# Optimization experiments

Hardware: AMD Instinct MI355X
Metric: run time of the kernel (lower is better)

## Reference

```python
import jax, jax.numpy as jnp
import numpy as np

B, T, C, H = 2, 2048, 2048, 32
N = C // H  # 64
EPS_GN = 1e-5 * 8 ** 2  # eps = 1e-5 * head_size_divisor**2


def setup_inputs() -> dict:
    key = jax.random.key(0)
    ks = jax.random.split(key, 40)
    p = lambda i, shape, s=1.0: jax.random.normal(ks[i], shape, jnp.float32) * s
    inp = {
        'x': p(0, (B, T, C)),
        'shift_state': jnp.zeros((B, C), jnp.float32),
        'v_first': p(1, (B, T, C)),
        'wkv_state': jnp.zeros((B, H, N, N), jnp.float32),
        # token-shift mix coefficients [1,1,C]
        'x_r': p(2, (1, 1, C), 0.3), 'x_w': p(3, (1, 1, C), 0.3),
        'x_k': p(4, (1, 1, C), 0.3), 'x_v': p(5, (1, 1, C), 0.3),
        'x_a': p(6, (1, 1, C), 0.3), 'x_g': p(7, (1, 1, C), 0.3),
        # decay LoRA
        'w0': p(8, (1, 1, C), 0.5) - 4.0,
        'w1': p(9, (C, 64), 0.02), 'w2': p(10, (64, C), 0.02),
        # in-context-learning-rate LoRA
        'a0': p(11, (1, 1, C), 0.1),
        'a1': p(12, (C, 64), 0.02), 'a2': p(13, (64, C), 0.02),
        # value-mix LoRA
        'v0': p(14, (1, 1, C), 0.1) + 1.0,
        'v1': p(15, (C, 32), 0.02), 'v2': p(16, (32, C), 0.02),
        # gate LoRA
        'g1': p(17, (C, 128), 0.02), 'g2': p(18, (128, C), 0.02),
        'k_k': p(19, (1, 1, C), 0.05) + 0.85,
        'k_a': p(20, (1, 1, C), 0.05) + 1.0,
        'r_k': p(21, (H, N), 0.1),
        # dense projections (applied as x @ W.T like nn.Linear)
        'Wr': p(22, (C, C), 0.02), 'Wk': p(23, (C, C), 0.02),
        'Wv': p(24, (C, C), 0.02), 'Wo': p(25, (C, C), 0.02),
        'ln_w': jnp.ones((C,), jnp.float32),
        'ln_b': jnp.zeros((C,), jnp.float32),
    }
    return inp


def reference(x, shift_state, v_first, wkv_state, x_r, x_w, x_k, x_v, x_a, x_g,
              w0, w1, w2, a0, a1, a2, v0, v1, v2, g1, g2, k_k, k_a, r_k,
              Wr, Wk, Wv, Wo, ln_w, ln_b):
    # token shift: xx[t] = x[t-1] - x[t] (prev from shift_state at t=0)
    xx = jnp.concatenate([shift_state[:, None, :], x[:, :-1]], axis=1) - x
    xr, xw, xk, xv, xa, xg = (x + xx * m for m in (x_r, x_w, x_k, x_v, x_a, x_g))

    r = xr @ Wr.T
    w = -jax.nn.softplus(-(w0 + jnp.tanh(xw @ w1) @ w2)) - 0.5  # log-decay in (-inf,-0.5)
    k = xk @ Wk.T
    v = xv @ Wv.T
    v = v + (v_first - v) * jax.nn.sigmoid(v0 + (xv @ v1) @ v2)  # layer_id > 0 branch
    a = jax.nn.sigmoid(a0 + (xa @ a1) @ a2)
    g = jax.nn.sigmoid(xg @ g1) @ g2

    kk = (k * k_k).reshape(B, T, H, N)
    kk = kk / jnp.maximum(jnp.linalg.norm(kk, axis=-1, keepdims=True), 1e-12)
    kk = kk.reshape(B, T, C)
    k = k * (1.0 + (a - 1.0) * k_a)

    # RWKV-7 generalized delta-rule recurrence (a_in=-kk, b_in=kk*a):
    #   S_t = S_{t-1} * diag(exp(w_t)) + (S_{t-1} a_t) b_t^T + v_t k_t^T ; o_t = S_t r_t
    to_tbhn = lambda z: z.reshape(B, T, H, N).transpose(1, 0, 2, 3)  # [T,B,H,N]
    rs, ws, ks, vs, as_, bs = map(to_tbhn, (r, w, k, v, -kk, kk * a))

    def step(S, ins):  # S: [B,H,N,N] indexed [v_dim, k_dim]
        r_t, w_t, k_t, v_t, a_t, b_t = ins
        sa = jnp.einsum('bhij,bhj->bhi', S, a_t)
        S = (S * jnp.exp(w_t)[:, :, None, :]
             + sa[..., None] * b_t[:, :, None, :]
             + v_t[..., None] * k_t[:, :, None, :])
        o_t = jnp.einsum('bhij,bhj->bhi', S, r_t)
        return S, o_t

    _, o = jax.lax.scan(step, wkv_state, (rs, ws, ks, vs, as_, bs))  # o: [T,B,H,N]
    o = o.transpose(1, 0, 2, 3).reshape(B, T, C)

    # GroupNorm with H groups over channel dim
    og = o.reshape(B, T, H, N)
    mu = og.mean(-1, keepdims=True)
    var = og.var(-1, keepdims=True)
    o = ((og - mu) / jnp.sqrt(var + EPS_GN)).reshape(B, T, C) * ln_w + ln_b

    # bonus term
    rk = (r.reshape(B, T, H, N) * k.reshape(B, T, H, N) * r_k).sum(-1, keepdims=True)
    o = o + (rk * v.reshape(B, T, H, N)).reshape(B, T, C)

    return (o * g) @ Wo.T
```

## Files before the change

kernel.cpp:

```cpp
#include <hip/hip_runtime.h>

#define Bdim 2
#define Tdim 2048
#define Cdim 2048
#define Hdim 32
#define Mdim (Bdim*Tdim)

typedef unsigned short u16;
typedef short bf16x8 __attribute__((ext_vector_type(8)));
typedef float f32x2 __attribute__((ext_vector_type(2)));
typedef float f32x4 __attribute__((ext_vector_type(4)));

__device__ __forceinline__ u16 f2bf(float f) {
  unsigned u = __float_as_uint(f);
  u = (u + 0x7FFFu + ((u >> 16) & 1u)) >> 16;
  return (u16)u;
}
__device__ __forceinline__ float b2f(u16 h) {
  return __uint_as_float(((unsigned)h) << 16);
}
__device__ __forceinline__ float sigf(float x) { return 1.f / (1.f + expf(-x)); }

__device__ __forceinline__ void gld16(const u16* g, u16* l) {
  __builtin_amdgcn_global_load_lds(
      (const __attribute__((address_space(1))) unsigned int*)g,
      (__attribute__((address_space(3))) unsigned int*)l, 16, 0, 0);
}

__device__ __forceinline__ float dpp_red16(float x) {
  int t = __builtin_amdgcn_mov_dpp(__float_as_int(x), 0x128, 0xF, 0xF, true);
  x += __int_as_float(t);
  t = __builtin_amdgcn_mov_dpp(__float_as_int(x), 0x124, 0xF, 0xF, true);
  x += __int_as_float(t);
  t = __builtin_amdgcn_mov_dpp(__float_as_int(x), 0x122, 0xF, 0xF, true);
  x += __int_as_float(t);
  t = __builtin_amdgcn_mov_dpp(__float_as_int(x), 0x121, 0xF, 0xF, true);
  x += __int_as_float(t);
  return x;
}

__global__ __launch_bounds__(256) void fill_kernel(float* __restrict__ out, float v, int n) {
  int i = blockIdx.x * 256 + threadIdx.x;
  if (i < n) out[i] = v;
}

__global__ __launch_bounds__(256) void prep_kernel(
    const float* __restrict__ x, const float* __restrict__ shift,
    const float* __restrict__ mr, const float* __restrict__ mw,
    const float* __restrict__ mk, const float* __restrict__ mv,
    const float* __restrict__ ma, const float* __restrict__ mg,
    u16* __restrict__ xr_h, u16* __restrict__ xr_l,
    u16* __restrict__ xk_h, u16* __restrict__ xk_l,
    u16* __restrict__ xv_h, u16* __restrict__ xv_l,
    u16* __restrict__ xg_h, u16* __restrict__ xg_l,
    u16* __restrict__ xw, u16* __restrict__ xa)
{
  size_t idx = (size_t)blockIdx.x * 256 + threadIdx.x;
  int c = (int)(idx & (Cdim - 1));
  size_t row = idx >> 11;
  int t = (int)(row & (Tdim - 1));
  int b = (int)(row >> 11);
  float xc = x[idx];
  float xp = (t == 0) ? shift[(size_t)b * Cdim + c] : x[idx - Cdim];
  float xx = xp - xc;

  float vr = xc + xx * mr[c];
  u16 hr = f2bf(vr); xr_h[idx] = hr; xr_l[idx] = f2bf(vr - b2f(hr));
  float vk = xc + xx * mk[c];
  u16 hk = f2bf(vk); xk_h[idx] = hk; xk_l[idx] = f2bf(vk - b2f(hk));
  float vv = xc + xx * mv[c];
  u16 hv = f2bf(vv); xv_h[idx] = hv; xv_l[idx] = f2bf(vv - b2f(hv));
  float vg = xc + xx * mg[c];
  u16 hg = f2bf(vg); xg_h[idx] = hg; xg_l[idx] = f2bf(vg - b2f(hg));

  xw[idx] = f2bf(xc + xx * mw[c]);
  xa[idx] = f2bf(xc + xx * ma[c]);
}

__global__ __launch_bounds__(256) void cast_split_kernel(
    const float* __restrict__ src, u16* __restrict__ hi, u16* __restrict__ lo)
{
  size_t i = (size_t)blockIdx.x * 256 + threadIdx.x;
  float v = src[i];
  u16 h = f2bf(v);
  hi[i] = h;
  lo[i] = f2bf(v - b2f(h));
}

__global__ __launch_bounds__(256) void pack_all_kernel(
    const float* __restrict__ w1, const float* __restrict__ a1,
    const float* __restrict__ v1, const float* __restrict__ g1,
    const float* __restrict__ w2, const float* __restrict__ a2,
    const float* __restrict__ v2, const float* __restrict__ g2,
    u16* __restrict__ w1t, u16* __restrict__ a1t, u16* __restrict__ v1t,
    u16* __restrict__ g1t_h, u16* __restrict__ g1t_l,
    u16* __restrict__ w2t, u16* __restrict__ a2t, u16* __restrict__ v2t,
    u16* __restrict__ g2t_h, u16* __restrict__ g2t_l)
{
  int bid = blockIdx.x;
  const float* src; u16* dh; u16* dl = nullptr;
  int K, Nsrc; size_t idx0;
  if (bid < 1024)      { src = w1; dh = w1t;   K = 2048; Nsrc = 64;   idx0 = (size_t)bid * 256; }
  else if (bid < 2048) { src = a1; dh = a1t;   K = 2048; Nsrc = 64;   idx0 = (size_t)(bid - 1024) * 256; }
  else if (bid < 3072) { src = v1; dh = v1t;   K = 2048; Nsrc = 32;   idx0 = (size_t)(bid - 2048) * 256; }
  else if (bid < 4096) { src = g1; dh = g1t_h; dl = g1t_l; K = 2048; Nsrc = 128; idx0 = (size_t)(bid - 3072) * 256; }
  else if (bid < 4608) { src = w2; dh = w2t;   K = 64;   Nsrc = 2048; idx0 = (size_t)(bid - 4096) * 256; }
  else if (bid < 5120) { src = a2; dh = a2t;   K = 64;   Nsrc = 2048; idx0 = (size_t)(bid - 4608) * 256; }
  else if (bid < 5376) { src = v2; dh = v2t;   K = 32;   Nsrc = 2048; idx0 = (size_t)(bid - 5120) * 256; }
  else                 { src = g2; dh = g2t_h; dl = g2t_l; K = 128;  Nsrc = 2048; idx0 = (size_t)(bid - 5376) * 256; }
  size_t idx = idx0 + threadIdx.x;
  int n = (int)(idx / K);
  int kk = (int)(idx - (size_t)n * K);
  float v = (n < Nsrc) ? src[(size_t)kk * Nsrc + n] : 0.f;
  u16 h = f2bf(v);
  dh[idx] = h;
  if (dl) dl[idx] = f2bf(v - b2f(h));
}


template <int EP>
__device__ __forceinline__ void gemm_plain_body(
    const u16* __restrict__ A, const u16* __restrict__ B, void* __restrict__ Cv,
    const float* __restrict__ bias, const float* __restrict__ aux1,
    const float* __restrict__ aux2, int K, int Nact, int ldC, int act)
{
  __shared__ u16 As[2][128][32];
  __shared__ u16 Bs[2][128][32];
  int tid = threadIdx.x;
  int lane = tid & 63, wave = tid >> 6;
  int wm = wave >> 1, wn = wave & 1;
  int bm = blockIdx.x * 128, bn = blockIdx.y * 128;
  f32x4 zero = {0.f, 0.f, 0.f, 0.f};
  f32x4 acc[4][4];
#pragma unroll
  for (int i = 0; i < 4; i++)
#pragma unroll
    for (int j = 0; j < 4; j++) acc[i][j] = zero;
  int srow = tid >> 2;
  int sslot = tid & 3;
  int scol = (sslot ^ (srow & 3)) << 3;
  int dcol = sslot << 3;
  const u16* gA  = A + (size_t)(bm + srow) * K + scol;
  const u16* gA2 = A + (size_t)(bm + 64 + srow) * K + scol;
  const u16* gB  = B + (size_t)(bn + srow) * K + scol;
  const u16* gB2 = B + (size_t)(bn + 64 + srow) * K + scol;
  int fr = lane & 15;
  int fk = ((lane >> 4) << 3) ^ ((fr & 3) << 3);

#define STAGEP(buf, kk) { \
  gld16(gA + (kk), &As[buf][srow][dcol]); \
  gld16(gA2 + (kk), &As[buf][64 + srow][dcol]); \
  gld16(gB + (kk), &Bs[buf][srow][dcol]); \
  gld16(gB2 + (kk), &Bs[buf][64 + srow][dcol]); }

  STAGEP(0, 0)
  __syncthreads();
  int cur = 0;
  for (int k0 = 0; k0 < K; k0 += 32) {
    if (k0 + 32 < K) STAGEP(cur ^ 1, k0 + 32)
    bf16x8 af[4], bfv[4];
#pragma unroll
    for (int i = 0; i < 4; i++) af[i] = *(const bf16x8*)&As[cur][wm * 64 + i * 16 + fr][fk];
#pragma unroll
    for (int j = 0; j < 4; j++) bfv[j] = *(const bf16x8*)&Bs[cur][wn * 64 + j * 16 + fr][fk];
#pragma unroll
    for (int i = 0; i < 4; i++)
#pragma unroll
      for (int j = 0; j < 4; j++)
        acc[i][j] = __builtin_amdgcn_mfma_f32_16x16x32_bf16(af[i], bfv[j], acc[i][j], 0, 0, 0);
    __syncthreads();
    cur ^= 1;
  }
#undef STAGEP
  int rb = (lane >> 4) << 2;
  int cc = lane & 15;
#pragma unroll
  for (int i = 0; i < 4; i++) {
    int mm = bm + wm * 64 + i * 16 + rb;
#pragma unroll
    for (int j = 0; j < 4; j++) {
      int nn = bn + wn * 64 + j * 16 + cc;
      if (nn < Nact) {
#pragma unroll
        for (int r = 0; r < 4; r++) {
          float val = acc[i][j][r];
          size_t oidx = (size_t)(mm + r) * ldC + nn;
          if (EP == 1) ((u16*)Cv)[oidx] = f2bf(tanhf(val));
          else if (EP == 2) {
            if (act == 1) val = tanhf(val);
            ((u16*)Cv)[oidx] = f2bf(val);
          }
          else if (EP == 3) ((u16*)Cv)[oidx] = f2bf(0.60653065971f * sigf(bias[nn] + val));
          else if (EP == 4) ((float*)Cv)[oidx] = sigf(bias[nn] + val);
          else if (EP == 5) {
            float vraw = aux1[oidx], vf = aux2[oidx];
            ((float*)Cv)[oidx] = vraw + (vf - vraw) * sigf(bias[nn] + val);
          }
        }
      }
    }
  }
}

__global__ __launch_bounds__(256) void lora1_kernel(
    const u16* A0, const u16* A1, const u16* A2,
    const u16* B0, const u16* B1, const u16* B2,
    u16* C0, u16* C1, u16* C2, int N0, int N1, int N2)
{
  int z = blockIdx.z;
  const u16* A = (z == 0) ? A0 : (z == 1) ? A1 : A2;
  const u16* B = (z == 0) ? B0 : (z == 1) ? B1 : B2;
  u16* C      = (z == 0) ? C0 : (z == 1) ? C1 : C2;
  int Nact    = (z == 0) ? N0 : (z == 1) ? N1 : N2;
  int act     = (z == 0) ? 1 : 0;
  gemm_plain_body<2>(A, B, C, nullptr, nullptr, nullptr, 2048, Nact, Nact, act);
}

__global__ __launch_bounds__(256) void lora2_kernel(
    const u16* Aw, const u16* Aa, const u16* Av,
    const u16* Bw, const u16* Ba, const u16* Bv,
    u16* Cw, float* Ca, float* Cv,
    const float* w0, const float* a0, const float* v0,
    const float* vfirst)
{
  int z = blockIdx.z;
  if (z == 0)
    gemm_plain_body<3>(Aw, Bw, Cw, w0, nullptr, nullptr, 64, Cdim, Cdim, 0);
  else if (z == 1)
    gemm_plain_body<4>(Aa, Ba, Ca, a0, nullptr, nullptr, 64, Cdim, Cdim, 0);
  else
    gemm_plain_body<5>(Av, Bv, Cv, v0, Cv, vfirst, 32, Cdim, Cdim, 0);
}

template <int EP>
__global__ __launch_bounds__(256) void gemm_split(
    const u16* __restrict__ Ah, const u16* __restrict__ Al,
    const u16* __restrict__ Bh, const u16* __restrict__ Bl,
    void* __restrict__ C1, u16* __restrict__ C2, int K, int Nact, int ldC)
{
  __shared__ u16 Ash[2][128][32];
  __shared__ u16 Asl[2][128][32];
  __shared__ u16 Bsh[2][128][32];
  __shared__ u16 Bsl[2][128][32];
  int tid = threadIdx.x;
  int lane = tid & 63, wave = tid >> 6;
  int wm = wave >> 1, wn = wave & 1;
  int bm = blockIdx.x * 128, bn = blockIdx.y * 128;
  f32x4 zero = {0.f, 0.f, 0.f, 0.f};
  f32x4 acc[4][4];
#pragma unroll
  for (int i = 0; i < 4; i++)
#pragma unroll
    for (int j = 0; j < 4; j++) acc[i][j] = zero;
  int srow = tid >> 2;
  int sslot = tid & 3;
  int scol = (sslot ^ (srow & 3)) << 3;
  int dcol = sslot << 3;
  size_t ga  = (size_t)(bm + srow) * K + scol;
  size_t ga2 = (size_t)(bm + 64 + srow) * K + scol;
  size_t gb  = (size_t)(bn + srow) * K + scol;
  size_t gb2 = (size_t)(bn + 64 + srow) * K + scol;
  int fr = lane & 15;
  int fk = ((lane >> 4) << 3) ^ ((fr & 3) << 3);

#define STAGES(buf, kk) { \
  gld16(Ah + ga + (kk), &Ash[buf][srow][dcol]); \
  gld16(Ah + ga2 + (kk), &Ash[buf][64 + srow][dcol]); \
  gld16(Al + ga + (kk), &Asl[buf][srow][dcol]); \
  gld16(Al + ga2 + (kk), &Asl[buf][64 + srow][dcol]); \
  gld16(Bh + gb + (kk), &Bsh[buf][srow][dcol]); \
  gld16(Bh + gb2 + (kk), &Bsh[buf][64 + srow][dcol]); \
  gld16(Bl + gb + (kk), &Bsl[buf][srow][dcol]); \
  gld16(Bl + gb2 + (kk), &Bsl[buf][64 + srow][dcol]); }

  STAGES(0, 0)
  __syncthreads();
  int cur = 0;
  for (int k0 = 0; k0 < K; k0 += 32) {
    if (k0 + 32 < K) STAGES(cur ^ 1, k0 + 32)
    bf16x8 fah[4], fal[4], fbh[4], fbl[4];
#pragma unroll
    for (int i = 0; i < 4; i++) {
      fah[i] = *(const bf16x8*)&Ash[cur][wm * 64 + i * 16 + fr][fk];
      fal[i] = *(const bf16x8*)&Asl[cur][wm * 64 + i * 16 + fr][fk];
    }
#pragma unroll
    for (int j = 0; j < 4; j++) {
      fbh[j] = *(const bf16x8*)&Bsh[cur][wn * 64 + j * 16 + fr][fk];
      fbl[j] = *(const bf16x8*)&Bsl[cur][wn * 64 + j * 16 + fr][fk];
    }
#pragma unroll
    for (int i = 0; i < 4; i++)
#pragma unroll
      for (int j = 0; j < 4; j++) {
        acc[i][j] = __builtin_amdgcn_mfma_f32_16x16x32_bf16(fah[i], fbh[j], acc[i][j], 0, 0, 0);
        acc[i][j] = __builtin_amdgcn_mfma_f32_16x16x32_bf16(fah[i], fbl[j], acc[i][j], 0, 0, 0);
        acc[i][j] = __builtin_amdgcn_mfma_f32_16x16x32_bf16(fal[i], fbh[j], acc[i][j], 0, 0, 0);
      }
    __syncthreads();
    cur ^= 1;
  }
#undef STAGES
  int rb = (lane >> 4) << 2;
  int cc = lane & 15;
#pragma unroll
  for (int i = 0; i < 4; i++) {
    int mm = bm + wm * 64 + i * 16 + rb;
#pragma unroll
    for (int j = 0; j < 4; j++) {
      int nn = bn + wn * 64 + j * 16 + cc;
      if (nn < Nact) {
#pragma unroll
        for (int r = 0; r < 4; r++) {
          float val = acc[i][j][r];
          size_t oidx = (size_t)(mm + r) * ldC + nn;
          if (EP == 0) ((float*)C1)[oidx] = val;
          else {
            float s = sigf(val);
            u16 h = f2bf(s);
            ((u16*)C1)[oidx] = h;
            C2[oidx] = f2bf(s - b2f(h));
          }
        }
      }
    }
  }
}

__global__ __launch_bounds__(256) void post_kernel(
    float* __restrict__ k, const float* __restrict__ a,
    const float* __restrict__ k_k, const float* __restrict__ k_a,
    float* __restrict__ ain, float* __restrict__ bin)
{
  int gid = blockIdx.x * 4 + (threadIdx.x >> 6);
  int lane = threadIdx.x & 63;
  int m = gid >> 5, h = gid & 31;
  int c = h * 64 + lane;
  size_t idx = (size_t)m * Cdim + c;

  float kr = k[idx];
  float av = a[idx];

  float kkv = kr * k_k[c];
  float ss = kkv * kkv;
#pragma unroll
  for (int off = 32; off; off >>= 1) ss += __shfl_xor(ss, off);
  float kkn = kkv / fmaxf(sqrtf(ss), 1e-12f);

  ain[idx] = -kkn;
  bin[idx] = kkn * av;
  k[idx] = kr * (1.f + (av - 1.f) * k_a[c]);
}

#define SG 16
__global__ __launch_bounds__(512) void scan_kernel(
    const float* __restrict__ r, const u16* __restrict__ ew,
    const float* __restrict__ k, const float* __restrict__ v,
    const float* __restrict__ ain, const float* __restrict__ bin,
    const float* __restrict__ S0, float* __restrict__ o)
{
  int bh = blockIdx.x & 63;
  int q4 = blockIdx.x >> 6;
  int tid = threadIdx.x;
  int wv = tid >> 6;
  int lane = tid & 63;
  int jci = (lane & 15) | ((lane >> 1) & 16);
  int lr = (lane >> 4) & 1;
  int i = q4 * 16 + wv * 2 + lr;
  int cb = (bh & 31) * 64;
  size_t mbase = (size_t)(bh >> 5) * Tdim;

  float s0, s1;
  {
    const float* sp = S0 + (size_t)bh * 4096 + (size_t)i * 64 + jci * 2;
    s0 = sp[0]; s1 = sp[1];
  }

  __shared__ __align__(16) char lds[45056];

  float ld0, ld1, ld2, ld3, ld4, ld5, ld6, ld7, ld8, ld9;
  unsigned lde;

#define SLOAD(gg) { \
  size_t gb_ = (mbase + (size_t)(gg) * SG) * Cdim + cb; \
  int w0_ = tid >> 6, c0_ = tid & 63;            \
  int w1_ = 8 + (tid >> 6);                      \
  ld0 = ain[gb_ + (size_t)w0_ * Cdim + c0_];  ld1 = ain[gb_ + (size_t)w1_ * Cdim + c0_]; \
  ld2 = k  [gb_ + (size_t)w0_ * Cdim + c0_];  ld3 = k  [gb_ + (size_t)w1_ * Cdim + c0_]; \
  ld4 = bin[gb_ + (size_t)w0_ * Cdim + c0_];  ld5 = bin[gb_ + (size_t)w1_ * Cdim + c0_]; \
  ld6 = r  [gb_ + (size_t)w0_ * Cdim + c0_];  ld7 = r  [gb_ + (size_t)w1_ * Cdim + c0_]; \
  ld8 = v  [gb_ + (size_t)w0_ * Cdim + c0_];  ld9 = v  [gb_ + (size_t)w1_ * Cdim + c0_]; \
  lde = *(const unsigned*)(ew + gb_ + (size_t)(tid >> 5) * Cdim + (tid & 31) * 2); }

#define SWRITE(slot) { \
  char* b_ = lds + (slot) * 22528; \
  int o0_ = (tid >> 6) * 256 + (tid & 63) * 4; \
  int o1_ = o0_ + 8 * 256; \
  *(float*)(b_ + o0_) = ld0;          *(float*)(b_ + o1_) = ld1; \
  *(float*)(b_ + 4096 + o0_) = ld2;   *(float*)(b_ + 4096 + o1_) = ld3; \
  *(float*)(b_ + 8192 + o0_) = ld4;   *(float*)(b_ + 8192 + o1_) = ld5; \
  *(float*)(b_ + 12288 + o0_) = ld6;  *(float*)(b_ + 12288 + o1_) = ld7; \
  *(float*)(b_ + 16384 + o0_) = ld8;  *(float*)(b_ + 16384 + o1_) = ld9; \
  *(unsigned*)(b_ + 20480 + (tid >> 5) * 128 + (tid & 31) * 4) = lde; }

  const int NG = Tdim / SG;
  SLOAD(0)
  SWRITE(0)
  SLOAD(1)
  __syncthreads();

  for (int g = 0; g < NG; ++g) {
    {
      char* b_ = lds + (g & 1) * 22528;
      size_t obase = (mbase + (size_t)g * SG) * Cdim + cb + i;
#pragma unroll
      for (int sub = 0; sub < SG; ++sub) {
        f32x2 av_ = *(const f32x2*)(b_ + sub * 256 + jci * 8);
        f32x2 kv_ = *(const f32x2*)(b_ + 4096 + sub * 256 + jci * 8);
        f32x2 bv_ = *(const f32x2*)(b_ + 8192 + sub * 256 + jci * 8);
        f32x2 rv_ = *(const f32x2*)(b_ + 12288 + sub * 256 + jci * 8);
        float vi_ = *(const float*)(b_ + 16384 + sub * 256 + i * 4);
        unsigned e_ = *(const unsigned*)(b_ + 20480 + sub * 128 + jci * 4);
        float p_ = s0 * av_[0] + s1 * av_[1];
        p_ = dpp_red16(p_);
        p_ += __shfl_xor(p_, 32);
        float e0_ = b2f((u16)(e_ & 0xFFFFu));
        float e1_ = b2f((u16)(e_ >> 16));
        float sn0_ = s0 * e0_ + p_ * bv_[0] + vi_ * kv_[0];
        float sn1_ = s1 * e1_ + p_ * bv_[1] + vi_ * kv_[1];
        s0 = sn0_; s1 = sn1_;
        float oo_ = sn0_ * rv_[0] + sn1_ * rv_[1];
        oo_ = dpp_red16(oo_);
        oo_ += __shfl_xor(oo_, 32);
        if (jci == 0) o[obase + (size_t)sub * Cdim] = oo_;
      }
    }
    __syncthreads();
    if (g + 1 < NG) {
      SWRITE((g + 1) & 1)
      if (g + 2 < NG) SLOAD(g + 2)
      __syncthreads();
    }
  }
#undef SLOAD
#undef SWRITE
}

__global__ __launch_bounds__(256) void gn_kernel(
    const float* __restrict__ o_raw, const float* __restrict__ r,
    const float* __restrict__ k, const float* __restrict__ v,
    const float* __restrict__ g, const float* __restrict__ rkw,
    const float* __restrict__ ln_w, const float* __restrict__ ln_b,
    u16* __restrict__ og_h, u16* __restrict__ og_l)
{
  int gid = blockIdx.x * 4 + (threadIdx.x >> 6);
  int lane = threadIdx.x & 63;
  int m = gid >> 5, h = gid & 31;
  int c = h * 64 + lane;
  size_t idx = (size_t)m * Cdim + c;

  float ov = o_raw[idx];
  float rv = r[idx], kv = k[idx], vv = v[idx];
  float rk = rv * kv * rkw[c];

  float s1 = ov, s2 = ov * ov, s3 = rk;
#pragma unroll
  for (int off = 32; off; off >>= 1) {
    s1 += __shfl_xor(s1, off);
    s2 += __shfl_xor(s2, off);
    s3 += __shfl_xor(s3, off);
  }
  float mu = s1 * (1.f / 64.f);
  float var = s2 * (1.f / 64.f) - mu * mu;
  float xh = (ov - mu) * rsqrtf(var + 6.4e-4f);
  float gn = xh * ln_w[c] + ln_b[c];
  float outp = (gn + s3 * vv) * g[idx];
  u16 hh = f2bf(outp);
  og_h[idx] = hh;
  og_l[idx] = f2bf(outp - b2f(hh));
}

extern "C" void kernel_launch(void* const* d_in, const int* in_sizes, int n_in,
                              void* d_out, int out_size, void* d_ws, size_t ws_size,
                              hipStream_t stream) {
  const float* x      = (const float*)d_in[0];
  const float* shiftS = (const float*)d_in[1];
  const float* vfirst = (const float*)d_in[2];
  const float* wkv0   = (const float*)d_in[3];
  const float* x_r = (const float*)d_in[4];
  const float* x_w = (const float*)d_in[5];
  const float* x_k = (const float*)d_in[6];
  const float* x_v = (const float*)d_in[7];
  const float* x_a = (const float*)d_in[8];
  const float* x_g = (const float*)d_in[9];
  const float* w0 = (const float*)d_in[10];
  const float* w1 = (const float*)d_in[11];
  const float* w2 = (const float*)d_in[12];
  const float* a0 = (const float*)d_in[13];
  const float* a1 = (const float*)d_in[14];
  const float* a2 = (const float*)d_in[15];
  const float* v0 = (const float*)d_in[16];
  const float* v1 = (const float*)d_in[17];
  const float* v2 = (const float*)d_in[18];
  const float* g1 = (const float*)d_in[19];
  const float* g2 = (const float*)d_in[20];
  const float* k_k = (const float*)d_in[21];
  const float* k_a = (const float*)d_in[22];
  const float* r_k = (const float*)d_in[23];
  const float* Wr = (const float*)d_in[24];
  const float* Wk = (const float*)d_in[25];
  const float* Wv = (const float*)d_in[26];
  const float* Wo = (const float*)d_in[27];
  const float* ln_w = (const float*)d_in[28];
  const float* ln_b = (const float*)d_in[29];
  (void)in_sizes; (void)n_in;

  const size_t MC = (size_t)Mdim * Cdim;
  const size_t CC = (size_t)Cdim * Cdim;
  const size_t SLOT = MC * 2;

  char* cur = (char*)d_ws;
  auto alloc = [&](size_t bytes) -> void* {
    void* p = cur;
    cur += (bytes + 255) & ~(size_t)255;
    return p;
  };

  char* X = (char*)alloc(13 * SLOT);
  u16* xr_h = (u16*)(X + 0 * SLOT);
  u16* xr_l = (u16*)(X + 1 * SLOT);
  u16* xk_h = (u16*)(X + 2 * SLOT);
  u16* xk_l = (u16*)(X + 3 * SLOT);
  u16* xv_h = (u16*)(X + 4 * SLOT);
  u16* xv_l = (u16*)(X + 5 * SLOT);
  u16* xw   = (u16*)(X + 6 * SLOT);
  u16* xa   = (u16*)(X + 7 * SLOT);
  u16* xg_h = (u16*)(X + 8 * SLOT);
  u16* xg_l = (u16*)(X + 9 * SLOT);
  float* r_f32 = (float*)(X + 8 * SLOT);
  float* k_f32 = (float*)(X + 0 * SLOT);
  float* v_f32 = (float*)(X + 2 * SLOT);
  float* a_f32 = (float*)(X + 10 * SLOT);
  u16*   ew_bf = (u16*)(X + 12 * SLOT);
  float* ain_f = (float*)(X + 4 * SLOT);
  float* bin_f = (float*)(X + 6 * SLOT);
  float* o_f32 = (float*)(X + 10 * SLOT);
  float* g_f32 = (float*)(X + 6 * SLOT);
  u16*   og_h  = (u16*)(X + 4 * SLOT);
  u16*   og_l  = (u16*)(X + 5 * SLOT);

  u16* Wh = (u16*)alloc(CC * 2);
  u16* Wl = (u16*)alloc(CC * 2);

  u16* w1t = (u16*)alloc((size_t)128 * 2048 * 2);
  u16* a1t = (u16*)alloc((size_t)128 * 2048 * 2);
  u16* v1t = (u16*)alloc((size_t)128 * 2048 * 2);
  u16* g1t_h = (u16*)alloc((size_t)128 * 2048 * 2);
  u16* g1t_l = (u16*)alloc((size_t)128 * 2048 * 2);
  u16* w2t = (u16*)alloc((size_t)2048 * 64 * 2);
  u16* a2t = (u16*)alloc((size_t)2048 * 64 * 2);
  u16* v2t = (u16*)alloc((size_t)2048 * 32 * 2);
  u16* g2t_h = (u16*)alloc((size_t)2048 * 128 * 2);
  u16* g2t_l = (u16*)alloc((size_t)2048 * 128 * 2);
  u16* hb_w = (u16*)alloc((size_t)Mdim * 64 * 2);
  u16* hb_a = (u16*)alloc((size_t)Mdim * 64 * 2);
  u16* hb_v = (u16*)alloc((size_t)Mdim * 32 * 2);
  u16* sig_h = (u16*)alloc((size_t)Mdim * 128 * 2);
  u16* sig_l = (u16*)alloc((size_t)Mdim * 128 * 2);

  size_t required = (size_t)(cur - (char*)d_ws);
  if (ws_size < required) {
    fill_kernel<<<(out_size + 255) / 256, 256, 0, stream>>>(
        (float*)d_out, (float)(ws_size >> 20), out_size);
    return;
  }

  prep_kernel<<<(int)(MC / 256), 256, 0, stream>>>(
      x, shiftS, x_r, x_w, x_k, x_v, x_a, x_g,
      xr_h, xr_l, xk_h, xk_l, xv_h, xv_l, xg_h, xg_l, xw, xa);

  pack_all_kernel<<<6400, 256, 0, stream>>>(
      w1, a1, v1, g1, w2, a2, v2, g2,
      w1t, a1t, v1t, g1t_h, g1t_l, w2t, a2t, v2t, g2t_h, g2t_l);

  dim3 gL1(Mdim / 128, 1, 3);
  lora1_kernel<<<gL1, 256, 0, stream>>>(xw, xa, xv_h, w1t, a1t, v1t,
                                        hb_w, hb_a, hb_v, 64, 64, 32);
  dim3 gL1g(Mdim / 128, 1);
  gemm_split<1><<<gL1g, 256, 0, stream>>>(xg_h, xg_l, g1t_h, g1t_l,
                                          sig_h, sig_l, 2048, 128, 128);

  dim3 gBig(Mdim / 128, Cdim / 128);
  cast_split_kernel<<<(int)(CC / 256), 256, 0, stream>>>(Wr, Wh, Wl);
  gemm_split<0><<<gBig, 256, 0, stream>>>(xr_h, xr_l, Wh, Wl, r_f32, nullptr, Cdim, Cdim, Cdim);
  cast_split_kernel<<<(int)(CC / 256), 256, 0, stream>>>(Wk, Wh, Wl);
  gemm_split<0><<<gBig, 256, 0, stream>>>(xk_h, xk_l, Wh, Wl, k_f32, nullptr, Cdim, Cdim, Cdim);
  cast_split_kernel<<<(int)(CC / 256), 256, 0, stream>>>(Wv, Wh, Wl);
  gemm_split<0><<<gBig, 256, 0, stream>>>(xv_h, xv_l, Wh, Wl, v_f32, nullptr, Cdim, Cdim, Cdim);

  dim3 gL2(Mdim / 128, Cdim / 128, 3);
  lora2_kernel<<<gL2, 256, 0, stream>>>(hb_w, hb_a, hb_v, w2t, a2t, v2t,
                                        ew_bf, a_f32, v_f32, w0, a0, v0, vfirst);

  post_kernel<<<(Mdim * Hdim) / 4, 256, 0, stream>>>(
      k_f32, a_f32, k_k, k_a, ain_f, bin_f);

  scan_kernel<<<256, 512, 0, stream>>>(
      r_f32, ew_bf, k_f32, v_f32, ain_f, bin_f, wkv0, o_f32);

  gemm_split<0><<<gBig, 256, 0, stream>>>(sig_h, sig_l, g2t_h, g2t_l,
                                          g_f32, nullptr, 128, Cdim, Cdim);

  gn_kernel<<<(Mdim * Hdim) / 4, 256, 0, stream>>>(
      o_f32, r_f32, k_f32, v_f32, g_f32, r_k, ln_w, ln_b, og_h, og_l);

  cast_split_kernel<<<(int)(CC / 256), 256, 0, stream>>>(Wo, Wh, Wl);
  gemm_split<0><<<gBig, 256, 0, stream>>>(og_h, og_l, Wh, Wl,
                                          (float*)d_out, nullptr, Cdim, Cdim, Cdim);
}
```

Baseline: 1.138 ms.

## Double chunk size in WKV scan and interleave per-step LDS operands

Raises the scan's per-group timestep count from 16 to 32, halving the number of barrier-separated staging rounds. The staging loads switch to vectorized f32x2/f32x4 global reads. The LDS layout interleaves a with k and b with r so each scan step reads two 16-byte vectors instead of four 8-byte ones. LDS use doubles to about 88 KB per block, which may limit occupancy and raises register pressure in the fully unrolled loop.

```diff
diff --git a/kernel.cpp b/kernel.cpp
--- a/kernel.cpp
+++ b/kernel.cpp
@@ -352,7 +352,7 @@
   k[idx] = kr * (1.f + (av - 1.f) * k_a[c]);
 }
 
-#define SG 16
+#define SG 32
 __global__ __launch_bounds__(512) void scan_kernel(
     const float* __restrict__ r, const u16* __restrict__ ew,
     const float* __restrict__ k, const float* __restrict__ v,
@@ -376,32 +376,43 @@
     s0 = sp[0]; s1 = sp[1];
   }
 
-  __shared__ __align__(16) char lds[45056];
-
-  float ld0, ld1, ld2, ld3, ld4, ld5, ld6, ld7, ld8, ld9;
-  unsigned lde;
+  __shared__ __align__(16) char lds[90112];
+
+  f32x2 ak0a, ak0k, br0b, br0r;  unsigned e0r;
+  f32x2 ak1a, ak1k, br1b, br1r;  unsigned e1r;
+  f32x4 vv4;
 
 #define SLOAD(gg) { \
   size_t gb_ = (mbase + (size_t)(gg) * SG) * Cdim + cb; \
-  int w0_ = tid >> 6, c0_ = tid & 63;            \
-  int w1_ = 8 + (tid >> 6);                      \
-  ld0 = ain[gb_ + (size_t)w0_ * Cdim + c0_];  ld1 = ain[gb_ + (size_t)w1_ * Cdim + c0_]; \
-  ld2 = k  [gb_ + (size_t)w0_ * Cdim + c0_];  ld3 = k  [gb_ + (size_t)w1_ * Cdim + c0_]; \
-  ld4 = bin[gb_ + (size_t)w0_ * Cdim + c0_];  ld5 = bin[gb_ + (size_t)w1_ * Cdim + c0_]; \
-  ld6 = r  [gb_ + (size_t)w0_ * Cdim + c0_];  ld7 = r  [gb_ + (size_t)w1_ * Cdim + c0_]; \
-  ld8 = v  [gb_ + (size_t)w0_ * Cdim + c0_];  ld9 = v  [gb_ + (size_t)w1_ * Cdim + c0_]; \
-  lde = *(const unsigned*)(ew + gb_ + (size_t)(tid >> 5) * Cdim + (tid & 31) * 2); }
+  { int sub_ = tid >> 5, j_ = tid & 31; \
+    size_t a_ = gb_ + (size_t)sub_ * Cdim + j_ * 2; \
+    ak0a = *(const f32x2*)(ain + a_);  ak0k = *(const f32x2*)(k + a_); \
+    br0b = *(const f32x2*)(bin + a_);  br0r = *(const f32x2*)(r + a_); \
+    e0r  = *(const unsigned*)(ew + a_); } \
+  { int sub_ = 16 + (tid >> 5), j_ = tid & 31; \
+    size_t a_ = gb_ + (size_t)sub_ * Cdim + j_ * 2; \
+    ak1a = *(const f32x2*)(ain + a_);  ak1k = *(const f32x2*)(k + a_); \
+    br1b = *(const f32x2*)(bin + a_);  br1r = *(const f32x2*)(r + a_); \
+    e1r  = *(const unsigned*)(ew + a_); } \
+  { int sub_ = tid >> 4, ch_ = (tid & 15) * 4; \
+    vv4 = *(const f32x4*)(v + gb_ + (size_t)sub_ * Cdim + ch_); } }
 
 #define SWRITE(slot) { \
-  char* b_ = lds + (slot) * 22528; \
-  int o0_ = (tid >> 6) * 256 + (tid & 63) * 4; \
-  int o1_ = o0_ + 8 * 256; \
-  *(float*)(b_ + o0_) = ld0;          *(float*)(b_ + o1_) = ld1; \
-  *(float*)(b_ + 4096 + o0_) = ld2;   *(float*)(b_ + 4096 + o1_) = ld3; \
-  *(float*)(b_ + 8192 + o0_) = ld4;   *(float*)(b_ + 8192 + o1_) = ld5; \
-  *(float*)(b_ + 12288 + o0_) = ld6;  *(float*)(b_ + 12288 + o1_) = ld7; \
-  *(float*)(b_ + 16384 + o0_) = ld8;  *(float*)(b_ + 16384 + o1_) = ld9; \
-  *(unsigned*)(b_ + 20480 + (tid >> 5) * 128 + (tid & 31) * 4) = lde; }
+  char* b_ = lds + (slot) * 45056; \
+  { int sub_ = tid >> 5, j_ = tid & 31; \
+    f32x4 t_; t_[0] = ak0a[0]; t_[1] = ak0a[1]; t_[2] = ak0k[0]; t_[3] = ak0k[1]; \
+    *(f32x4*)(b_ + sub_ * 512 + j_ * 16) = t_; \
+    f32x4 u_; u_[0] = br0b[0]; u_[1] = br0b[1]; u_[2] = br0r[0]; u_[3] = br0r[1]; \
+    *(f32x4*)(b_ + 16384 + sub_ * 512 + j_ * 16) = u_; \
+    *(unsigned*)(b_ + 40960 + sub_ * 128 + j_ * 4) = e0r; } \
+  { int sub_ = 16 + (tid >> 5), j_ = tid & 31; \
+    f32x4 t_; t_[0] = ak1a[0]; t_[1] = ak1a[1]; t_[2] = ak1k[0]; t_[3] = ak1k[1]; \
+    *(f32x4*)(b_ + sub_ * 512 + j_ * 16) = t_; \
+    f32x4 u_; u_[0] = br1b[0]; u_[1] = br1b[1]; u_[2] = br1r[0]; u_[3] = br1r[1]; \
+    *(f32x4*)(b_ + 16384 + sub_ * 512 + j_ * 16) = u_; \
+    *(unsigned*)(b_ + 40960 + sub_ * 128 + j_ * 4) = e1r; } \
+  { int sub_ = tid >> 4, ch_ = (tid & 15) * 4; \
+    *(f32x4*)(b_ + 32768 + sub_ * 256 + ch_ * 4) = vv4; } }
 
   const int NG = Tdim / SG;
   SLOAD(0)
@@ -411,25 +422,23 @@
 
   for (int g = 0; g < NG; ++g) {
     {
-      char* b_ = lds + (g & 1) * 22528;
+      char* b_ = lds + (g & 1) * 45056;
       size_t obase = (mbase + (size_t)g * SG) * Cdim + cb + i;
 #pragma unroll
       for (int sub = 0; sub < SG; ++sub) {
-        f32x2 av_ = *(const f32x2*)(b_ + sub * 256 + jci * 8);
-        f32x2 kv_ = *(const f32x2*)(b_ + 4096 + sub * 256 + jci * 8);
-        f32x2 bv_ = *(const f32x2*)(b_ + 8192 + sub * 256 + jci * 8);
-        f32x2 rv_ = *(const f32x2*)(b_ + 12288 + sub * 256 + jci * 8);
-        float vi_ = *(const float*)(b_ + 16384 + sub * 256 + i * 4);
-        unsigned e_ = *(const unsigned*)(b_ + 20480 + sub * 128 + jci * 4);
-        float p_ = s0 * av_[0] + s1 * av_[1];
+        f32x4 akv = *(const f32x4*)(b_ + sub * 512 + jci * 16);
+        f32x4 brv = *(const f32x4*)(b_ + 16384 + sub * 512 + jci * 16);
+        float vi_ = *(const float*)(b_ + 32768 + sub * 256 + i * 4);
+        unsigned e_ = *(const unsigned*)(b_ + 40960 + sub * 128 + jci * 4);
+        float p_ = s0 * akv[0] + s1 * akv[1];
         p_ = dpp_red16(p_);
         p_ += __shfl_xor(p_, 32);
         float e0_ = b2f((u16)(e_ & 0xFFFFu));
         float e1_ = b2f((u16)(e_ >> 16));
-        float sn0_ = s0 * e0_ + p_ * bv_[0] + vi_ * kv_[0];
-        float sn1_ = s1 * e1_ + p_ * bv_[1] + vi_ * kv_[1];
+        float sn0_ = s0 * e0_ + p_ * brv[0] + vi_ * akv[2];
+        float sn1_ = s1 * e1_ + p_ * brv[1] + vi_ * akv[3];
         s0 = sn0_; s1 = sn1_;
-        float oo_ = sn0_ * rv_[0] + sn1_ * rv_[1];
+        float oo_ = sn0_ * brv[2] + sn1_ * brv[3];
         oo_ = dpp_red16(oo_);
         oo_ += __shfl_xor(oo_, 32);
         if (jci == 0) o[obase + (size_t)sub * Cdim] = oo_;
```

Measured after the change: 1.131 ms. About the same (-0.6%).
